# Kernel optimization log

Measured on AMD Instinct MI355X. Metric: run time of the kernel, lower is better.

Reference implementation:

```python
import jax, jax.numpy as jnp
import numpy as np

IN_C = 32        # in_channel
CH = IN_C + 3    # first-layer input channel (use_coords=True)
HID = 8
OUT_C = 1
# parameter slicing offsets: w1(35*8) b1(8) w2(8*8) b2(8) w3(8*1) b3(1) = 369
P_COUNT = CH * HID + HID + HID * HID + HID + HID * OUT_C + OUT_C


def setup_inputs() -> dict:
    key = jax.random.key(0)
    k1, k2, k3, k4 = jax.random.split(key, 4)
    num_prop, num_all = 128, 100000
    prop_feats = jax.random.normal(k1, (num_prop, IN_C), dtype=jnp.float32)
    all_features = jax.random.normal(k2, (num_all, CH), dtype=jnp.float32)
    W_dyn = jax.random.normal(k3, (IN_C, P_COUNT), dtype=jnp.float32) * 0.05
    b_dyn = jax.random.normal(k4, (P_COUNT,), dtype=jnp.float32) * 0.05
    return {"prop_feats": prop_feats, "all_features": all_features,
            "W_dyn": W_dyn, "b_dyn": b_dyn}


def reference(prop_feats, all_features, W_dyn, b_dyn):
    P = prop_feats.shape[0]
    params = prop_feats @ W_dyn + b_dyn  # (P, 369)
    s = 0
    def take(n):
        nonlocal s
        out = params[:, s:s + n]
        s += n
        return out
    w1 = take(CH * HID).reshape(P, CH, HID)
    b1 = take(HID)[:, None, :]
    w2 = take(HID * HID).reshape(P, HID, HID)
    b2 = take(HID)[:, None, :]
    w3 = take(HID * OUT_C).reshape(P, HID, OUT_C)
    b3 = take(OUT_C)[:, None, :]
    # layer 1: shared all_features against per-proposal weights (avoids
    # materializing the (P, A, CH) expanded tensor)
    f = jax.nn.relu(jnp.einsum('ac,pch->pah', all_features, w1) + b1)
    # layer 2
    f = jax.nn.relu(jnp.einsum('pah,phk->pak', f, w2) + b2)
    # layer 3 (no activation on last kernel)
    f = jnp.einsum('pah,pho->pao', f, w3) + b3
    return f  # (num_prop, num_all, out_channel)
```

## Files before the change

### kernel.cpp

```cpp
#include <hip/hip_runtime.h>
#include <hip/hip_bf16.h>

#define IN_C  32
#define CH    35
#define P_CNT 369
#define NPAIR 64
#define NALL  100000
#define NTILE 6250
#define PP    4
#define NWX   256

#define OW1 0
#define OB1 280
#define OW2 288
#define OB2 352
#define OW3 360
#define OB3 368

#define WS_W1F 0
#define WS_W2F 131072
#define WS_B2F 229376
#define WS_W3F 294912
#define WS_B3F 360448
#define WS_A3F 360960

typedef short  bf16x8 __attribute__((ext_vector_type(8)));
typedef short  bf16x4 __attribute__((ext_vector_type(4)));
typedef float  f32x4  __attribute__((ext_vector_type(4)));

static __device__ inline unsigned short f2bf(float x) {
    union { float f; unsigned u; } v; v.f = x;
    unsigned r = v.u + 0x7FFFu + ((v.u >> 16) & 1u);
    return (unsigned short)(r >> 16);
}

static __device__ inline unsigned pack2bf(float lo, float hi) {
    __hip_bfloat162 h2 = __float22bfloat162_rn(make_float2(lo, hi));
    union { __hip_bfloat162 h; unsigned u; } c; c.h = h2; return c.u;
}

__global__ __launch_bounds__(256) void prep_kernel(
        const float* __restrict__ prop,
        const float* __restrict__ W,
        const float* __restrict__ b,
        char* __restrict__ ws) {
    const int pp  = blockIdx.x;
    const int tid = threadIdx.x;
    __shared__ float P[2][P_CNT];

    for (int idx = tid; idx < 2 * P_CNT; idx += 256) {
        const int pl = (idx >= P_CNT) ? 1 : 0;
        const int j  = idx - pl * P_CNT;
        const float* pr = prop + (size_t)(2 * pp + pl) * IN_C;
        float acc = b[j];
        #pragma unroll
        for (int c = 0; c < IN_C; ++c)
            acc = fmaf(pr[c], W[(size_t)c * P_CNT + j], acc);
        P[pl][j] = acc;
    }
    __syncthreads();

    if (tid >= 64) return;
    const int lane = tid;
    const int g = lane >> 4;
    const int m = lane & 15;

    {
        unsigned short* w1f = (unsigned short*)(ws + WS_W1F);
        const int pl = m >> 3, h = m & 7;
        #pragma unroll
        for (int kh = 0; kh < 2; ++kh)
            #pragma unroll
            for (int j = 0; j < 8; ++j) {
                const int c = kh * 32 + g * 8 + j;
                float v = 0.f;
                if (c < CH) v = P[pl][OW1 + c * 8 + h];
                else if (c == CH) v = P[pl][OB1 + h];
                w1f[((size_t)(pp * 2 + kh) * 64 + lane) * 8 + j] = f2bf(v);
            }
    }
    {
        unsigned short* w2f = (unsigned short*)(ws + WS_W2F);
        const int plj = m >> 3, jj = m & 7;
        #pragma unroll
        for (int r = 0; r < 4; ++r) {
            const int colh = g * 4 + r;
            const int ph = colh >> 3, h = colh & 7;
            const float v = (ph == plj) ? P[plj][OW2 + h * 8 + jj] : 0.f;
            w2f[((size_t)pp * 64 + lane) * 4 + r] = f2bf(v);
        }
    }
    {
        unsigned short* a3f = (unsigned short*)(ws + WS_A3F);
        #pragma unroll
        for (int r = 0; r < 4; ++r) {
            const int kg = g * 4 + r;
            float v = 0.f;
            if (m == 0 && kg < 8)  v = P[0][OW3 + kg];
            if (m == 8 && kg >= 8) v = P[1][OW3 + kg - 8];
            a3f[((size_t)pp * 64 + lane) * 4 + r] = f2bf(v);
        }
    }
    {
        float* b2f = (float*)(ws + WS_B2F);
        float* w3f = (float*)(ws + WS_W3F);
        #pragma unroll
        for (int r = 0; r < 4; ++r) {
            const int row = g * 4 + r;
            b2f[((size_t)pp * 64 + lane) * 4 + r] = P[row >> 3][OB2 + (row & 7)];
            w3f[((size_t)pp * 64 + lane) * 4 + r] = P[row >> 3][OW3 + (row & 7)];
        }
    }
    if (lane < 2) ((float*)(ws + WS_B3F))[pp * 2 + lane] = P[lane][OB3];
}

#define LOAD_TILE(T, O0, O1) do {                                             \
    const float* fr_ = allf + (size_t)((T) * 16 + col) * CH;                  \
    const float v0_ = fr_[g * 8 + 0], v1_ = fr_[g * 8 + 1];                   \
    const float v2_ = fr_[g * 8 + 2], v3_ = fr_[g * 8 + 3];                   \
    const float v4_ = fr_[g * 8 + 4], v5_ = fr_[g * 8 + 5];                   \
    const float v6_ = fr_[g * 8 + 6], v7_ = fr_[g * 8 + 7];                   \
    float e0_ = 0.f, e1_ = 0.f, e2_ = 0.f, e3_ = 0.f;                         \
    if (g == 0) { e0_ = fr_[32]; e1_ = fr_[33]; e2_ = fr_[34]; e3_ = 1.f; }   \
    union { unsigned u[4]; bf16x8 v; } A0_, A1_;                              \
    A0_.u[0] = pack2bf(v0_, v1_); A0_.u[1] = pack2bf(v2_, v3_);               \
    A0_.u[2] = pack2bf(v4_, v5_); A0_.u[3] = pack2bf(v6_, v7_);               \
    A1_.u[0] = pack2bf(e0_, e1_); A1_.u[1] = pack2bf(e2_, e3_);               \
    A1_.u[2] = 0u; A1_.u[3] = 0u;                                             \
    O0 = A0_.v; O1 = A1_.v; } while (0)

__global__ __launch_bounds__(256, 4) void mlp_kernel(
        const float* __restrict__ allf,
        const char* __restrict__ ws,
        float* __restrict__ out) {
    const int lane = threadIdx.x & 63;
    const int wave = threadIdx.x >> 6;
    const int wx   = blockIdx.x * 4 + wave;
    const int g    = lane >> 4;
    const int col  = lane & 15;
    const int ppbase = blockIdx.y * PP;

    const bf16x8* __restrict__ w1f = (const bf16x8*)(ws + WS_W1F);
    const bf16x4* __restrict__ w2f = (const bf16x4*)(ws + WS_W2F);
    const bf16x4* __restrict__ a3f = (const bf16x4*)(ws + WS_A3F);
    const f32x4*  __restrict__ b2f = (const f32x4*)(ws + WS_B2F);
    const float*  __restrict__ b3f = (const float*)(ws + WS_B3F);

    bf16x8 w1a[PP], w1b[PP];
    bf16x4 w2v[PP], a3v[PP];
    f32x4  b2v[PP], b3v[PP];
    #pragma unroll
    for (int i = 0; i < PP; ++i) {
        const int pp = ppbase + i;
        w1a[i] = w1f[(pp * 2 + 0) * 64 + lane];
        w1b[i] = w1f[(pp * 2 + 1) * 64 + lane];
        w2v[i] = w2f[pp * 64 + lane];
        a3v[i] = a3f[pp * 64 + lane];
        b2v[i] = b2f[pp * 64 + lane];
        const float b3e = b3f[pp * 2 + 0], b3o = b3f[pp * 2 + 1];
        b3v[i] = (f32x4){ (g == 0) ? b3e : ((g == 2) ? b3o : 0.f), 0.f, 0.f, 0.f };
    }
    #pragma unroll
    for (int i = 0; i < PP; ++i)
        asm volatile("" : "+v"(w1a[i]), "+v"(w1b[i]), "+v"(w2v[i]),
                          "+v"(a3v[i]), "+v"(b2v[i]), "+v"(b3v[i]));

    if (wx >= NTILE) return;

    bf16x8 cb0, cb1, nb0, nb1;
    LOAD_TILE(wx, cb0, cb1);

    #pragma unroll 1
    for (int t = wx; t < NTILE; t += NWX) {
        const int tn = (t + NWX < NTILE) ? (t + NWX) : t;
        LOAD_TILE(tn, nb0, nb1);

        #pragma unroll
        for (int i = 0; i < PP; ++i) {
            f32x4 c1 = {0.f, 0.f, 0.f, 0.f};
            c1 = __builtin_amdgcn_mfma_f32_16x16x32_bf16(w1a[i], cb0, c1, 0, 0, 0);
            c1 = __builtin_amdgcn_mfma_f32_16x16x32_bf16(w1b[i], cb1, c1, 0, 0, 0);

#if __has_builtin(__builtin_amdgcn_mfma_f32_16x16x16bf16_1k)
            union { unsigned u[2]; bf16x4 v; } pb;
            pb.u[0] = pack2bf(fmaxf(c1[0], 0.f), fmaxf(c1[1], 0.f));
            pb.u[1] = pack2bf(fmaxf(c1[2], 0.f), fmaxf(c1[3], 0.f));
            f32x4 c2 = __builtin_amdgcn_mfma_f32_16x16x16bf16_1k(w2v[i], pb.v, b2v[i], 0, 0, 0);

            union { unsigned u[2]; bf16x4 v; } pc;
            pc.u[0] = pack2bf(fmaxf(c2[0], 0.f), fmaxf(c2[1], 0.f));
            pc.u[1] = pack2bf(fmaxf(c2[2], 0.f), fmaxf(c2[3], 0.f));
            f32x4 c3 = __builtin_amdgcn_mfma_f32_16x16x16bf16_1k(a3v[i], pc.v, b3v[i], 0, 0, 0);

            if (!(g & 1)) {
                const int pl = lane >> 5;
                out[(size_t)((ppbase + i) * 2 + pl) * NALL + t * 16 + col] = c3[0];
            }
#else
            const f32x4 w3vv = ((const f32x4*)(ws + WS_W3F))[(ppbase + i) * 64 + lane];
            float rl[4];
            #pragma unroll
            for (int r = 0; r < 4; ++r) rl[r] = fmaxf(c1[r], 0.f);
            bf16x8 pb8;
            #pragma unroll
            for (int j = 0; j < 8; ++j) {
                const int src = ((2 * g + (j >> 2)) << 4) + col;
                pb8[j] = (short)f2bf(__shfl(rl[j & 3], src, 64));
            }
            bf16x8 w28;
            #pragma unroll
            for (int r = 0; r < 4; ++r) { w28[r] = w2v[i][r]; w28[r + 4] = 0; }
            f32x4 c2 = __builtin_amdgcn_mfma_f32_16x16x32_bf16(w28, pb8, b2v[i], 0, 0, 0);
            float s;
            s = fmaf(fmaxf(c2[0], 0.f), w3vv[0], 0.f);
            s = fmaf(fmaxf(c2[1], 0.f), w3vv[1], s);
            s = fmaf(fmaxf(c2[2], 0.f), w3vv[2], s);
            s = fmaf(fmaxf(c2[3], 0.f), w3vv[3], s);
            const float tv = s + __shfl_xor(s, 16, 64);
            if (!(g & 1)) {
                const int pl = lane >> 5;
                out[(size_t)((ppbase + i) * 2 + pl) * NALL + t * 16 + col] =
                    tv + b3f[(ppbase + i) * 2 + pl];
            }
#endif
        }
        cb0 = nb0; cb1 = nb1;
    }
}

extern "C" void kernel_launch(void* const* d_in, const int* in_sizes, int n_in,
                              void* d_out, int out_size, void* d_ws, size_t ws_size,
                              hipStream_t stream) {
    const float* prop = (const float*)d_in[0];
    const float* allf = (const float*)d_in[1];
    const float* W    = (const float*)d_in[2];
    const float* b    = (const float*)d_in[3];
    float* out = (float*)d_out;
    char*  ws  = (char*)d_ws;

    prep_kernel<<<NPAIR, 256, 0, stream>>>(prop, W, b, ws);

    dim3 grid(64, NPAIR / PP);
    mlp_kernel<<<grid, 256, 0, stream>>>(allf, ws, out);
}
```

Measured before the change: 128.9 us.

## Pre-convert features to bf16 MFMA layout once and double the grid

Adds a prep kernel that converts all_features into bf16 fragments already in MFMA operand layout and stores them in the workspace. The MLP kernel then does vector loads of those fragments instead of 35 strided fp32 loads and conversions per tile, repeated for every proposal group. The MLP loop now interleaves two proposals' MFMA chains for ILP and adds b3 after the last MFMA. The grid is doubled to 128 blocks in x. This costs an extra kernel launch and a workspace write/read pass, and it depends on the workspace being large enough, with a fallback path otherwise.

```diff
diff --git a/kernel.cpp b/kernel.cpp
--- a/kernel.cpp
+++ b/kernel.cpp
@@ -8,7 +8,7 @@
 #define NALL  100000
 #define NTILE 6250
 #define PP    4
-#define NWX   256
+#define NWX   512
 
 #define OW1 0
 #define OB1 280
@@ -23,10 +23,22 @@
 #define WS_W3F 294912
 #define WS_B3F 360448
 #define WS_A3F 360960
+#define WS_F0  524288
+#define WS_F1  6924288
+#define WS_NEED 7724288
 
 typedef short  bf16x8 __attribute__((ext_vector_type(8)));
 typedef short  bf16x4 __attribute__((ext_vector_type(4)));
 typedef float  f32x4  __attribute__((ext_vector_type(4)));
+typedef unsigned u32x2 __attribute__((ext_vector_type(2)));
+
+#define MFMA32 __builtin_amdgcn_mfma_f32_16x16x32_bf16
+#if __has_builtin(__builtin_amdgcn_mfma_f32_16x16x16bf16_1k)
+#define HAVE_1K 1
+#define MFMA16 __builtin_amdgcn_mfma_f32_16x16x16bf16_1k
+#else
+#define HAVE_1K 0
+#endif
 
 static __device__ inline unsigned short f2bf(float x) {
     union { float f; unsigned u; } v; v.f = x;
@@ -114,7 +126,27 @@
     if (lane < 2) ((float*)(ws + WS_B3F))[pp * 2 + lane] = P[lane][OB3];
 }
 
-#define LOAD_TILE(T, O0, O1) do {                                             \
+__global__ __launch_bounds__(256) void prep_feat(
+        const float* __restrict__ allf, char* __restrict__ ws) {
+    const int lane = threadIdx.x & 63;
+    const int tile = blockIdx.x * 4 + (threadIdx.x >> 6);
+    if (tile >= NTILE) return;
+    const int g = lane >> 4, col = lane & 15;
+    const float* fr = allf + (size_t)(tile * 16 + col) * CH;
+    union { unsigned u[4]; bf16x8 v; } A;
+    A.u[0] = pack2bf(fr[g * 8 + 0], fr[g * 8 + 1]);
+    A.u[1] = pack2bf(fr[g * 8 + 2], fr[g * 8 + 3]);
+    A.u[2] = pack2bf(fr[g * 8 + 4], fr[g * 8 + 5]);
+    A.u[3] = pack2bf(fr[g * 8 + 6], fr[g * 8 + 7]);
+    ((bf16x8*)(ws + WS_F0))[(size_t)tile * 64 + lane] = A.v;
+    if (g == 0) {
+        unsigned* dst = (unsigned*)(ws + WS_F1) + ((size_t)tile * 16 + col) * 2;
+        dst[0] = pack2bf(fr[32], fr[33]);
+        dst[1] = pack2bf(fr[34], 1.0f);
+    }
+}
+
+#define LOAD_TILE_FB(T, O0, O1) do {                                          \
     const float* fr_ = allf + (size_t)((T) * 16 + col) * CH;                  \
     const float v0_ = fr_[g * 8 + 0], v1_ = fr_[g * 8 + 1];                   \
     const float v2_ = fr_[g * 8 + 2], v3_ = fr_[g * 8 + 3];                   \
@@ -129,13 +161,18 @@
     A1_.u[2] = 0u; A1_.u[3] = 0u;                                             \
     O0 = A0_.v; O1 = A1_.v; } while (0)
 
+#define BUILD_HI(E, O1) do {                                                  \
+    union { unsigned u[4]; bf16x8 v; } B_;                                    \
+    B_.u[0] = (g == 0) ? (E)[0] : 0u; B_.u[1] = (g == 0) ? (E)[1] : 0u;       \
+    B_.u[2] = 0u; B_.u[3] = 0u; O1 = B_.v; } while (0)
+
+template<bool PRE>
 __global__ __launch_bounds__(256, 4) void mlp_kernel(
         const float* __restrict__ allf,
         const char* __restrict__ ws,
         float* __restrict__ out) {
     const int lane = threadIdx.x & 63;
-    const int wave = threadIdx.x >> 6;
-    const int wx   = blockIdx.x * 4 + wave;
+    const int wx   = blockIdx.x * 4 + (threadIdx.x >> 6);
     const int g    = lane >> 4;
     const int col  = lane & 15;
     const int ppbase = blockIdx.y * PP;
@@ -145,10 +182,13 @@
     const bf16x4* __restrict__ a3f = (const bf16x4*)(ws + WS_A3F);
     const f32x4*  __restrict__ b2f = (const f32x4*)(ws + WS_B2F);
     const float*  __restrict__ b3f = (const float*)(ws + WS_B3F);
+    const bf16x8* __restrict__ f0  = (const bf16x8*)(ws + WS_F0);
+    const u32x2*  __restrict__ f1  = (const u32x2*)(ws + WS_F1);
 
     bf16x8 w1a[PP], w1b[PP];
     bf16x4 w2v[PP], a3v[PP];
-    f32x4  b2v[PP], b3v[PP];
+    f32x4  b2v[PP];
+    float  b3s[PP];
     #pragma unroll
     for (int i = 0; i < PP; ++i) {
         const int pp = ppbase + i;
@@ -157,46 +197,65 @@
         w2v[i] = w2f[pp * 64 + lane];
         a3v[i] = a3f[pp * 64 + lane];
         b2v[i] = b2f[pp * 64 + lane];
-        const float b3e = b3f[pp * 2 + 0], b3o = b3f[pp * 2 + 1];
-        b3v[i] = (f32x4){ (g == 0) ? b3e : ((g == 2) ? b3o : 0.f), 0.f, 0.f, 0.f };
-    }
-    #pragma unroll
-    for (int i = 0; i < PP; ++i)
-        asm volatile("" : "+v"(w1a[i]), "+v"(w1b[i]), "+v"(w2v[i]),
-                          "+v"(a3v[i]), "+v"(b2v[i]), "+v"(b3v[i]));
-
-    if (wx >= NTILE) return;
-
-    bf16x8 cb0, cb1, nb0, nb1;
-    LOAD_TILE(wx, cb0, cb1);
+        b3s[i] = b3f[pp * 2 + (lane >> 5)];
+    }
+
+    bf16x8 cb0, cb1, pf0, pf1;
+    u32x2  pfe;
+    if (PRE) {
+        cb0 = f0[(size_t)wx * 64 + lane];
+        u32x2 e = f1[(size_t)wx * 16 + col];
+        BUILD_HI(e, cb1);
+    } else {
+        LOAD_TILE_FB(wx, cb0, cb1);
+    }
 
     #pragma unroll 1
     for (int t = wx; t < NTILE; t += NWX) {
         const int tn = (t + NWX < NTILE) ? (t + NWX) : t;
-        LOAD_TILE(tn, nb0, nb1);
-
+        if (PRE) {
+            pf0 = f0[(size_t)tn * 64 + lane];
+            pfe = f1[(size_t)tn * 16 + col];
+        } else {
+            LOAD_TILE_FB(tn, pf0, pf1);
+        }
+
+#if HAVE_1K
+        #pragma unroll
+        for (int q = 0; q < 2; ++q) {
+            const int i0 = 2 * q, i1 = 2 * q + 1;
+            f32x4 z = {0.f, 0.f, 0.f, 0.f};
+            f32x4 c1a = z, c1b = z;
+            c1a = MFMA32(w1a[i0], cb0, c1a, 0, 0, 0);
+            c1b = MFMA32(w1a[i1], cb0, c1b, 0, 0, 0);
+            c1a = MFMA32(w1b[i0], cb1, c1a, 0, 0, 0);
+            c1b = MFMA32(w1b[i1], cb1, c1b, 0, 0, 0);
+            union { unsigned u[2]; bf16x4 v; } pba, pbb;
+            pba.u[0] = pack2bf(fmaxf(c1a[0], 0.f), fmaxf(c1a[1], 0.f));
+            pbb.u[0] = pack2bf(fmaxf(c1b[0], 0.f), fmaxf(c1b[1], 0.f));
+            pba.u[1] = pack2bf(fmaxf(c1a[2], 0.f), fmaxf(c1a[3], 0.f));
+            pbb.u[1] = pack2bf(fmaxf(c1b[2], 0.f), fmaxf(c1b[3], 0.f));
+            f32x4 c2a = MFMA16(w2v[i0], pba.v, b2v[i0], 0, 0, 0);
+            f32x4 c2b = MFMA16(w2v[i1], pbb.v, b2v[i1], 0, 0, 0);
+            union { unsigned u[2]; bf16x4 v; } pca, pcb;
+            pca.u[0] = pack2bf(fmaxf(c2a[0], 0.f), fmaxf(c2a[1], 0.f));
+            pcb.u[0] = pack2bf(fmaxf(c2b[0], 0.f), fmaxf(c2b[1], 0.f));
+            pca.u[1] = pack2bf(fmaxf(c2a[2], 0.f), fmaxf(c2a[3], 0.f));
+            pcb.u[1] = pack2bf(fmaxf(c2b[2], 0.f), fmaxf(c2b[3], 0.f));
+            f32x4 c3a = MFMA16(a3v[i0], pca.v, z, 0, 0, 0);
+            f32x4 c3b = MFMA16(a3v[i1], pcb.v, z, 0, 0, 0);
+            if (!(g & 1)) {
+                const int pl = lane >> 5;
+                out[(size_t)((ppbase + i0) * 2 + pl) * NALL + t * 16 + col] = c3a[0] + b3s[i0];
+                out[(size_t)((ppbase + i1) * 2 + pl) * NALL + t * 16 + col] = c3b[0] + b3s[i1];
+            }
+        }
+#else
         #pragma unroll
         for (int i = 0; i < PP; ++i) {
             f32x4 c1 = {0.f, 0.f, 0.f, 0.f};
-            c1 = __builtin_amdgcn_mfma_f32_16x16x32_bf16(w1a[i], cb0, c1, 0, 0, 0);
-            c1 = __builtin_amdgcn_mfma_f32_16x16x32_bf16(w1b[i], cb1, c1, 0, 0, 0);
-
-#if __has_builtin(__builtin_amdgcn_mfma_f32_16x16x16bf16_1k)
-            union { unsigned u[2]; bf16x4 v; } pb;
-            pb.u[0] = pack2bf(fmaxf(c1[0], 0.f), fmaxf(c1[1], 0.f));
-            pb.u[1] = pack2bf(fmaxf(c1[2], 0.f), fmaxf(c1[3], 0.f));
-            f32x4 c2 = __builtin_amdgcn_mfma_f32_16x16x16bf16_1k(w2v[i], pb.v, b2v[i], 0, 0, 0);
-
-            union { unsigned u[2]; bf16x4 v; } pc;
-            pc.u[0] = pack2bf(fmaxf(c2[0], 0.f), fmaxf(c2[1], 0.f));
-            pc.u[1] = pack2bf(fmaxf(c2[2], 0.f), fmaxf(c2[3], 0.f));
-            f32x4 c3 = __builtin_amdgcn_mfma_f32_16x16x16bf16_1k(a3v[i], pc.v, b3v[i], 0, 0, 0);
-
-            if (!(g & 1)) {
-                const int pl = lane >> 5;
-                out[(size_t)((ppbase + i) * 2 + pl) * NALL + t * 16 + col] = c3[0];
-            }
-#else
+            c1 = MFMA32(w1a[i], cb0, c1, 0, 0, 0);
+            c1 = MFMA32(w1b[i], cb1, c1, 0, 0, 0);
             const f32x4 w3vv = ((const f32x4*)(ws + WS_W3F))[(ppbase + i) * 64 + lane];
             float rl[4];
             #pragma unroll
@@ -210,7 +269,7 @@
             bf16x8 w28;
             #pragma unroll
             for (int r = 0; r < 4; ++r) { w28[r] = w2v[i][r]; w28[r + 4] = 0; }
-            f32x4 c2 = __builtin_amdgcn_mfma_f32_16x16x32_bf16(w28, pb8, b2v[i], 0, 0, 0);
+            f32x4 c2 = MFMA32(w28, pb8, b2v[i], 0, 0, 0);
             float s;
             s = fmaf(fmaxf(c2[0], 0.f), w3vv[0], 0.f);
             s = fmaf(fmaxf(c2[1], 0.f), w3vv[1], s);
@@ -219,12 +278,12 @@
             const float tv = s + __shfl_xor(s, 16, 64);
             if (!(g & 1)) {
                 const int pl = lane >> 5;
-                out[(size_t)((ppbase + i) * 2 + pl) * NALL + t * 16 + col] =
-                    tv + b3f[(ppbase + i) * 2 + pl];
+                out[(size_t)((ppbase + i) * 2 + pl) * NALL + t * 16 + col] = tv + b3s[i];
             }
+        }
 #endif
-        }
-        cb0 = nb0; cb1 = nb1;
+        cb0 = pf0;
+        if (PRE) { BUILD_HI(pfe, cb1); } else { cb1 = pf1; }
     }
 }
 
@@ -240,6 +299,11 @@
 
     prep_kernel<<<NPAIR, 256, 0, stream>>>(prop, W, b, ws);
 
-    dim3 grid(64, NPAIR / PP);
-    mlp_kernel<<<grid, 256, 0, stream>>>(allf, ws, out);
-}
+    dim3 grid(128, NPAIR / PP);
+    if (ws_size >= (size_t)WS_NEED) {
+        prep_feat<<<(NTILE + 3) / 4, 256, 0, stream>>>(allf, ws);
+        mlp_kernel<true><<<grid, 256, 0, stream>>>(allf, ws, out);
+    } else {
+        mlp_kernel<false><<<grid, 256, 0, stream>>>(allf, ws, out);
+    }
+}
```

New measurement: 122.9 us. -4.7%, faster.
